# Kernel tuning notes

Measured on AMD Instinct MI355X. Metric: run time of the kernel, lower is better.

The kernel has to match this reference:

```python
import jax, jax.numpy as jnp
import numpy as np

TEMPERATURE = 0.1
NORMALIZE = True


def setup_inputs() -> dict:
    key = jax.random.key(0)
    k1, k2 = jax.random.split(key)
    B, D = 4096, 512
    return {
        "z_i": jax.random.normal(k1, (B, D), dtype=jnp.float32),
        "z_j": jax.random.normal(k2, (B, D), dtype=jnp.float32),
    }


def _l2norm(x):
    return x / jnp.sqrt(jnp.sum(x * x, axis=-1, keepdims=True))


def reference(z_i, z_j):
    if NORMALIZE:
        z_i = _l2norm(z_i)
        z_j = _l2norm(z_j)
    B = z_i.shape[0]

    inv_t = 1.0 / TEMPERATURE
    logits_aa = (z_i @ z_i.T) * inv_t  # [B, B]
    logits_bb = (z_j @ z_j.T) * inv_t
    logits_ab = (z_i @ z_j.T) * inv_t
    logits_ba = (z_j @ z_i.T) * inv_t

    # Static off-diagonal column indices: row i keeps cols 0..B-1 except i,
    # in ascending order (matches torch boolean-mask row-major extraction).
    j = jnp.arange(B - 1)[None, :]
    i = jnp.arange(B)[:, None]
    idx = j + (j >= i)  # [B, B-1] int32

    take = lambda m: jnp.take_along_axis(m, idx, axis=1)  # [B, B-1]

    pos = jnp.concatenate([jnp.diagonal(logits_ab), jnp.diagonal(logits_ba)])[:, None]  # [2B, 1]
    neg_a = jnp.concatenate([take(logits_aa), take(logits_ab)], axis=1)  # [B, 2(B-1)]
    neg_b = jnp.concatenate([take(logits_ba), take(logits_bb)], axis=1)
    neg = jnp.concatenate([neg_a, neg_b], axis=0)  # [2B, 2(B-1)]

    logits = jnp.concatenate([pos, neg], axis=1)  # [2B, 2B-1]
    logp = jax.nn.log_softmax(logits, axis=1)
    # Original forward uses labels = torch.ones(2B).long() -> target class 1.
    loss = -jnp.mean(logp[:, 1])
    return loss
```

## Files before the change

kernel.cpp:

```cpp
#include <hip/hip_runtime.h>
#include <hip/hip_bf16.h>


#define BB 4096
#define DD 512
#define NN 8192
#define TILE 128
#define KC 64
#define NBLK 2080

typedef __attribute__((ext_vector_type(8))) short short8;
typedef __attribute__((ext_vector_type(4))) float f32x4;

#define AS1 __attribute__((address_space(1)))
#define AS3 __attribute__((address_space(3)))
static __device__ __forceinline__ void gload_lds16(const void* g, void* l) {
    __builtin_amdgcn_global_load_lds((const AS1 void*)g, (AS3 void*)l, 16, 0, 0);
}

__global__ __launch_bounds__(256)
void normalize_kernel(const float* __restrict__ zi, const float* __restrict__ zj,
                      __hip_bfloat16* __restrict__ M, float* __restrict__ rowsum) {
    const int wave = threadIdx.x >> 6;
    const int lane = threadIdx.x & 63;
    const int row  = blockIdx.x * 4 + wave;
    if (threadIdx.x < 4) rowsum[blockIdx.x * 4 + threadIdx.x] = 0.f;
    const float* src = (row < BB) ? (zi + (size_t)row * DD)
                                  : (zj + (size_t)(row - BB) * DD);
    float4 v0 = ((const float4*)src)[lane * 2 + 0];
    float4 v1 = ((const float4*)src)[lane * 2 + 1];
    float ss = v0.x*v0.x + v0.y*v0.y + v0.z*v0.z + v0.w*v0.w
             + v1.x*v1.x + v1.y*v1.y + v1.z*v1.z + v1.w*v1.w;
    #pragma unroll
    for (int off = 1; off <= 32; off <<= 1) ss += __shfl_xor(ss, off);
    const float inv = rsqrtf(ss);
    short8 o;
    o[0] = (short)__bfloat16_as_ushort(__float2bfloat16(v0.x * inv));
    o[1] = (short)__bfloat16_as_ushort(__float2bfloat16(v0.y * inv));
    o[2] = (short)__bfloat16_as_ushort(__float2bfloat16(v0.z * inv));
    o[3] = (short)__bfloat16_as_ushort(__float2bfloat16(v0.w * inv));
    o[4] = (short)__bfloat16_as_ushort(__float2bfloat16(v1.x * inv));
    o[5] = (short)__bfloat16_as_ushort(__float2bfloat16(v1.y * inv));
    o[6] = (short)__bfloat16_as_ushort(__float2bfloat16(v1.z * inv));
    o[7] = (short)__bfloat16_as_ushort(__float2bfloat16(v1.w * inv));
    ((short8*)(M + (size_t)row * DD))[lane] = o;
}

__global__ __launch_bounds__(256, 4)
void gram_lse_kernel(const __hip_bfloat16* __restrict__ Mb,
                     float* __restrict__ rowsum, float* __restrict__ targets) {
    __shared__ __align__(16) short As[TILE * KC];
    __shared__ __align__(16) short Bs[TILE * KC];

    const int p = blockIdx.x;
    int by = (int)((sqrtf(8.0f * (float)p + 1.0f) - 1.0f) * 0.5f);
    while ((by + 1) * (by + 2) / 2 <= p) ++by;
    while (by * (by + 1) / 2 > p) --by;
    const int bx = p - by * (by + 1) / 2;

    const int rowBase = bx * TILE;
    const int colBase = by * TILE;
    const bool diag = (bx == by);
    const int tid  = threadIdx.x;
    const int wave = tid >> 6;
    const int lane = tid & 63;
    const int wr = (wave >> 1) * 64;
    const int wc = (wave & 1) * 64;
    const int l15 = lane & 15;
    const int l4  = lane >> 4;

    const short* Mg = (const short*)Mb;
    const short8* BsR = diag ? (const short8*)As : (const short8*)Bs;

    const int sg  = (tid & 7) ^ ((tid >> 3) & 7);
    const int sr0 = tid >> 3;
    const short* gA0 = Mg + (size_t)(rowBase + sr0) * DD + sg * 8;
    const short* gB0 = Mg + (size_t)(colBase + sr0) * DD + sg * 8;
    short* lA0 = As + tid * 8;
    short* lB0 = Bs + tid * 8;

    f32x4 acc[4][4] = {};

    for (int k0 = 0; k0 < DD; k0 += KC) {
        __syncthreads();
        #pragma unroll
        for (int i = 0; i < 4; ++i)
            gload_lds16(gA0 + k0 + (size_t)i * 32 * DD, lA0 + i * 2048);
        if (!diag) {
            #pragma unroll
            for (int i = 0; i < 4; ++i)
                gload_lds16(gB0 + k0 + (size_t)i * 32 * DD, lB0 + i * 2048);
        }
        __syncthreads();
        #pragma unroll
        for (int ks = 0; ks < KC / 32; ++ks) {
            const int gk = ks * 4 + l4;
            short8 a[4], b[4];
            #pragma unroll
            for (int mi = 0; mi < 4; ++mi) {
                int row = wr + mi * 16 + l15;
                a[mi] = ((const short8*)As)[row * 8 + (gk ^ (row & 7))];
            }
            #pragma unroll
            for (int ni = 0; ni < 4; ++ni) {
                int row = wc + ni * 16 + l15;
                b[ni] = BsR[row * 8 + (gk ^ (row & 7))];
            }
            #pragma unroll
            for (int mi = 0; mi < 4; ++mi)
                #pragma unroll
                for (int ni = 0; ni < 4; ++ni)
                    acc[mi][ni] = __builtin_amdgcn_mfma_f32_16x16x32_bf16(
                        a[mi], b[ni], acc[mi][ni], 0, 0, 0);
        }
    }

    float cs[4] = {0.f, 0.f, 0.f, 0.f};
    #pragma unroll
    for (int mi = 0; mi < 4; ++mi) {
        float rs[4] = {0.f, 0.f, 0.f, 0.f};
        #pragma unroll
        for (int ni = 0; ni < 4; ++ni) {
            const int gcol = colBase + wc + ni * 16 + l15;
            #pragma unroll
            for (int r = 0; r < 4; ++r) {
                const int grow = rowBase + wr + mi * 16 + l4 * 4 + r;
                float logit = 10.f * acc[mi][ni][r];
                float e = __expf(logit - 10.f);
                if (grow == gcol) e = 0.f;
                rs[r] += e;
                cs[ni] += e;
                if (rowBase == 0 && grow < 2) {
                    const int j0 = ((gcol & (BB - 1)) == 0) ? 1 : 0;
                    if (grow == j0) targets[gcol] = logit;
                }
            }
        }
        #pragma unroll
        for (int m = 1; m <= 8; m <<= 1)
            #pragma unroll
            for (int r = 0; r < 4; ++r)
                rs[r] += __shfl_xor(rs[r], m);
        if (l15 == 0) {
            #pragma unroll
            for (int r = 0; r < 4; ++r)
                atomicAdd(&rowsum[rowBase + wr + mi * 16 + l4 * 4 + r], rs[r]);
        }
    }
    if (!diag) {
        #pragma unroll
        for (int ni = 0; ni < 4; ++ni) {
            cs[ni] += __shfl_xor(cs[ni], 16);
            cs[ni] += __shfl_xor(cs[ni], 32);
        }
        if (l4 == 0) {
            #pragma unroll
            for (int ni = 0; ni < 4; ++ni)
                atomicAdd(&rowsum[colBase + wc + ni * 16 + l15], cs[ni]);
        }
    }
}

__global__ __launch_bounds__(256)
void finalize_kernel(const float* __restrict__ rowsum,
                     const float* __restrict__ targets, float* __restrict__ out) {
    const int tid = threadIdx.x;
    float s = 0.f;
    for (int t = tid; t < NN; t += 256)
        s += targets[t] - 10.f - __logf(rowsum[t]);
    #pragma unroll
    for (int off = 32; off; off >>= 1) s += __shfl_down(s, off);
    __shared__ float red[4];
    if ((tid & 63) == 0) red[tid >> 6] = s;
    __syncthreads();
    if (tid == 0) out[0] = -(red[0] + red[1] + red[2] + red[3]) / (float)NN;
}

extern "C" void kernel_launch(void* const* d_in, const int* in_sizes, int n_in,
                              void* d_out, int out_size, void* d_ws, size_t ws_size,
                              hipStream_t stream) {
    const float* zi = (const float*)d_in[0];
    const float* zj = (const float*)d_in[1];

    __hip_bfloat16* M = (__hip_bfloat16*)d_ws;
    float* rowsum  = (float*)((char*)d_ws + (size_t)NN * DD * 2);
    float* targets = rowsum + NN;
    float* out = (float*)d_out;

    normalize_kernel<<<NN / 4, 256, 0, stream>>>(zi, zj, M, rowsum);
    gram_lse_kernel<<<NBLK, 256, 0, stream>>>(M, rowsum, targets);
    finalize_kernel<<<1, 256, 0, stream>>>(rowsum, targets, out);
}
```

Before: 123.5 us.

## Switch Gram matrix to FP8 E4M3 MFMA with swizzled block order

Normalized embeddings are now quantized to FP8 E4M3 instead of bf16, and the Gram kernel uses the fp8 16x16x32 MFMA with a 128-byte K chunk, halving global and LDS traffic per element and doubling matrix throughput. Block indices are remapped across 8 groups to change the scheduling and L2 locality of triangle tiles. The finalize kernel now uses 1024 threads. FP8 quantization cuts precision in logits scaled by 10, which risks loss accuracy.

```diff
diff --git a/kernel.cpp b/kernel.cpp
--- a/kernel.cpp
+++ b/kernel.cpp
@@ -1,15 +1,15 @@
 #include <hip/hip_runtime.h>
 #include <hip/hip_bf16.h>
+#include <hip/hip_fp8.h>
 
 
 #define BB 4096
 #define DD 512
 #define NN 8192
 #define TILE 128
-#define KC 64
+#define KB 128
 #define NBLK 2080
 
-typedef __attribute__((ext_vector_type(8))) short short8;
 typedef __attribute__((ext_vector_type(4))) float f32x4;
 
 #define AS1 __attribute__((address_space(1)))
@@ -20,7 +20,7 @@
 
 __global__ __launch_bounds__(256)
 void normalize_kernel(const float* __restrict__ zi, const float* __restrict__ zj,
-                      __hip_bfloat16* __restrict__ M, float* __restrict__ rowsum) {
+                      unsigned char* __restrict__ M, float* __restrict__ rowsum) {
     const int wave = threadIdx.x >> 6;
     const int lane = threadIdx.x & 63;
     const int row  = blockIdx.x * 4 + wave;
@@ -34,25 +34,23 @@
     #pragma unroll
     for (int off = 1; off <= 32; off <<= 1) ss += __shfl_xor(ss, off);
     const float inv = rsqrtf(ss);
-    short8 o;
-    o[0] = (short)__bfloat16_as_ushort(__float2bfloat16(v0.x * inv));
-    o[1] = (short)__bfloat16_as_ushort(__float2bfloat16(v0.y * inv));
-    o[2] = (short)__bfloat16_as_ushort(__float2bfloat16(v0.z * inv));
-    o[3] = (short)__bfloat16_as_ushort(__float2bfloat16(v0.w * inv));
-    o[4] = (short)__bfloat16_as_ushort(__float2bfloat16(v1.x * inv));
-    o[5] = (short)__bfloat16_as_ushort(__float2bfloat16(v1.y * inv));
-    o[6] = (short)__bfloat16_as_ushort(__float2bfloat16(v1.z * inv));
-    o[7] = (short)__bfloat16_as_ushort(__float2bfloat16(v1.w * inv));
-    ((short8*)(M + (size_t)row * DD))[lane] = o;
+    const float vals[8] = {v0.x*inv, v0.y*inv, v0.z*inv, v0.w*inv,
+                           v1.x*inv, v1.y*inv, v1.z*inv, v1.w*inv};
+    union { long u; unsigned char b[8]; } pk;
+    #pragma unroll
+    for (int j = 0; j < 8; ++j)
+        pk.b[j] = __hip_cvt_float_to_fp8(vals[j], __HIP_SATFINITE, __HIP_E4M3);
+    ((long*)(M + (size_t)row * DD))[lane] = pk.u;
 }
 
 __global__ __launch_bounds__(256, 4)
-void gram_lse_kernel(const __hip_bfloat16* __restrict__ Mb,
+void gram_lse_kernel(const unsigned char* __restrict__ Mg,
                      float* __restrict__ rowsum, float* __restrict__ targets) {
-    __shared__ __align__(16) short As[TILE * KC];
-    __shared__ __align__(16) short Bs[TILE * KC];
+    __shared__ __align__(16) char As[TILE * KB];
+    __shared__ __align__(16) char Bs[TILE * KB];
 
-    const int p = blockIdx.x;
+    const int d = blockIdx.x;
+    const int p = (d & 7) * 260 + (d >> 3);
     int by = (int)((sqrtf(8.0f * (float)p + 1.0f) - 1.0f) * 0.5f);
     while ((by + 1) * (by + 2) / 2 <= p) ++by;
     while (by * (by + 1) / 2 > p) --by;
@@ -69,48 +67,47 @@
     const int l15 = lane & 15;
     const int l4  = lane >> 4;
 
-    const short* Mg = (const short*)Mb;
-    const short8* BsR = diag ? (const short8*)As : (const short8*)Bs;
-
     const int sg  = (tid & 7) ^ ((tid >> 3) & 7);
     const int sr0 = tid >> 3;
-    const short* gA0 = Mg + (size_t)(rowBase + sr0) * DD + sg * 8;
-    const short* gB0 = Mg + (size_t)(colBase + sr0) * DD + sg * 8;
-    short* lA0 = As + tid * 8;
-    short* lB0 = Bs + tid * 8;
+    const unsigned char* gA0 = Mg + (size_t)(rowBase + sr0) * DD + sg * 16;
+    const unsigned char* gB0 = Mg + (size_t)(colBase + sr0) * DD + sg * 16;
+    char* lA0 = As + tid * 16;
+    char* lB0 = Bs + tid * 16;
+
+    const int r7 = l15 & 7;
+    const int qh = l4 >> 1, ql = l4 & 1;
+    const int aoff0 = (wr + l15) * KB + ql * 8;
+    const int boff0 = (wc + l15) * KB + ql * 8;
+    const char* BsP = diag ? As : Bs;
 
     f32x4 acc[4][4] = {};
 
-    for (int k0 = 0; k0 < DD; k0 += KC) {
+    for (int k0 = 0; k0 < DD; k0 += KB) {
         __syncthreads();
         #pragma unroll
         for (int i = 0; i < 4; ++i)
-            gload_lds16(gA0 + k0 + (size_t)i * 32 * DD, lA0 + i * 2048);
+            gload_lds16(gA0 + k0 + (size_t)i * 32 * DD, lA0 + i * 4096);
         if (!diag) {
             #pragma unroll
             for (int i = 0; i < 4; ++i)
-                gload_lds16(gB0 + k0 + (size_t)i * 32 * DD, lB0 + i * 2048);
+                gload_lds16(gB0 + k0 + (size_t)i * 32 * DD, lB0 + i * 4096);
         }
         __syncthreads();
         #pragma unroll
-        for (int ks = 0; ks < KC / 32; ++ks) {
-            const int gk = ks * 4 + l4;
-            short8 a[4], b[4];
+        for (int ks = 0; ks < 4; ++ks) {
+            const int so = ((((ks << 1) | qh) ^ r7) << 4);
+            long a[4], b[4];
             #pragma unroll
-            for (int mi = 0; mi < 4; ++mi) {
-                int row = wr + mi * 16 + l15;
-                a[mi] = ((const short8*)As)[row * 8 + (gk ^ (row & 7))];
-            }
+            for (int mi = 0; mi < 4; ++mi)
+                a[mi] = *(const long*)(As + aoff0 + mi * 2048 + so);
             #pragma unroll
-            for (int ni = 0; ni < 4; ++ni) {
-                int row = wc + ni * 16 + l15;
-                b[ni] = BsR[row * 8 + (gk ^ (row & 7))];
-            }
+            for (int ni = 0; ni < 4; ++ni)
+                b[ni] = *(const long*)(BsP + boff0 + ni * 2048 + so);
             #pragma unroll
             for (int mi = 0; mi < 4; ++mi)
                 #pragma unroll
                 for (int ni = 0; ni < 4; ++ni)
-                    acc[mi][ni] = __builtin_amdgcn_mfma_f32_16x16x32_bf16(
+                    acc[mi][ni] = __builtin_amdgcn_mfma_f32_16x16x32_fp8_fp8(
                         a[mi], b[ni], acc[mi][ni], 0, 0, 0);
         }
     }
@@ -161,19 +158,25 @@
     }
 }
 
-__global__ __launch_bounds__(256)
+__global__ __launch_bounds__(1024)
 void finalize_kernel(const float* __restrict__ rowsum,
                      const float* __restrict__ targets, float* __restrict__ out) {
     const int tid = threadIdx.x;
     float s = 0.f;
-    for (int t = tid; t < NN; t += 256)
+    #pragma unroll
+    for (int t = tid; t < NN; t += 1024)
         s += targets[t] - 10.f - __logf(rowsum[t]);
     #pragma unroll
-    for (int off = 32; off; off >>= 1) s += __shfl_down(s, off);
-    __shared__ float red[4];
+    for (int off = 1; off <= 32; off <<= 1) s += __shfl_xor(s, off);
+    __shared__ float red[16];
     if ((tid & 63) == 0) red[tid >> 6] = s;
     __syncthreads();
-    if (tid == 0) out[0] = -(red[0] + red[1] + red[2] + red[3]) / (float)NN;
+    if (tid == 0) {
+        float t = 0.f;
+        #pragma unroll
+        for (int i = 0; i < 16; ++i) t += red[i];
+        out[0] = -t / (float)NN;
+    }
 }
 
 extern "C" void kernel_launch(void* const* d_in, const int* in_sizes, int n_in,
@@ -182,12 +185,12 @@
     const float* zi = (const float*)d_in[0];
     const float* zj = (const float*)d_in[1];
 
-    __hip_bfloat16* M = (__hip_bfloat16*)d_ws;
-    float* rowsum  = (float*)((char*)d_ws + (size_t)NN * DD * 2);
+    unsigned char* M = (unsigned char*)d_ws;
+    float* rowsum  = (float*)((char*)d_ws + (size_t)NN * DD);
     float* targets = rowsum + NN;
     float* out = (float*)d_out;
 
     normalize_kernel<<<NN / 4, 256, 0, stream>>>(zi, zj, M, rowsum);
     gram_lse_kernel<<<NBLK, 256, 0, stream>>>(M, rowsum, targets);
-    finalize_kernel<<<1, 256, 0, stream>>>(rowsum, targets, out);
+    finalize_kernel<<<1, 1024, 0, stream>>>(rowsum, targets, out);
 }
```

Result: faster. 100.7 us (-18.4%).
